# Optimization experiments

Measured on AMD Instinct MI355X. Metric: run time of the kernel, lower is better.

## Reference

```python
import jax, jax.numpy as jnp
import numpy as np

B, C, N, K = 8, 192, 3136, 9
COUT = 384


def setup_inputs() -> dict:
    key = jax.random.key(0)
    k1, k2, k3, k4 = jax.random.split(key, 4)
    x = jax.random.normal(k1, (B, C, N, 1), dtype=jnp.float32)
    edge_index = jax.random.randint(k2, (2, B, N, K), 0, N, dtype=jnp.int64)
    # 1x1 conv params: BasicConv([2C, COUT]) with bias, act='relu'
    W = jax.random.normal(k3, (COUT, 2 * C), dtype=jnp.float32) * (1.0 / np.sqrt(2 * C))
    b = jax.random.normal(k4, (COUT,), dtype=jnp.float32) * 0.01
    return {"x": x, "edge_index": edge_index, "W": W, "b": b}


def _gather(xs, idx):
    # xs: [B, C, N]; idx: [B, N, K] -> [B, C, N, K]
    return jax.vmap(lambda xb, ib: xb[:, ib])(xs, idx)


def reference(x, edge_index, W, b):
    xs = x[..., 0]                       # [B, C, N]
    x_i = _gather(xs, edge_index[1])     # [B, C, N, K] center features
    x_j = _gather(xs, edge_index[0])     # [B, C, N, K] neighbor features
    feat = jnp.concatenate([x_i, x_j - x_i], axis=1)  # [B, 2C, N, K]
    # 1x1 conv + bias + relu
    h = jnp.einsum('oi,bink->bonk', W, feat) + b[None, :, None, None]
    h = jax.nn.relu(h)                   # [B, COUT, N, K]
    return jnp.max(h, axis=-1, keepdims=True)  # [B, COUT, N, 1]
```

## Files before the change

### kernel.cpp

```cpp
#include <hip/hip_runtime.h>
#include <hip/hip_bf16.h>


#define Bb   8
#define Cc   192
#define Nn   3136
#define Kk   9
#define CO   384
#define TWOC 384
#define JTOT 768

typedef short  short8 __attribute__((ext_vector_type(8)));
typedef float  f32x4  __attribute__((ext_vector_type(4)));

__device__ __forceinline__ float bf2f(unsigned int u16) {
    union { unsigned int i; float f; } c;
    c.i = u16 << 16;
    return c.f;
}
__device__ __forceinline__ short f2bf(float f) {
    __hip_bfloat16 h = __float2bfloat16(f);
    short s; __builtin_memcpy(&s, &h, 2); return s;
}

__global__ __launch_bounds__(64) void detect(const unsigned short* __restrict__ xu,
                                             const int* __restrict__ ei,
                                             int* __restrict__ flags) {
    const int lane = threadIdx.x;
    unsigned int u = xu[2 * lane];
    int bige = (((u >> 7) & 0xFFu) >= 0x88u);
    unsigned long long bf = __ballot(bige);
    int oddnz = (ei[2 * lane + 1] != 0);
    unsigned long long bo = __ballot(oddnz);
    if (lane == 0) {
        flags[0] = (bf != 0ull) ? 1 : 0;
        flags[1] = (bo == 0ull) ? 1 : 0;
    }
}

__global__ __launch_bounds__(256) void prep_AT(const void* __restrict__ W_,
                                               short* __restrict__ A_Tb,
                                               const int* __restrict__ flags) {
    const int fp32 = flags[0];
    int t = blockIdx.x * 256 + threadIdx.x;
    if (t >= JTOT * Cc) return;
    int j = t / Cc;
    int c = t - j * Cc;
    int row = (j < CO) ? j : (j - CO);
    float w1, w2;
    if (fp32) {
        const float* W = (const float*)W_;
        w1 = W[row * TWOC + c];  w2 = W[row * TWOC + Cc + c];
    } else {
        const unsigned short* W = (const unsigned short*)W_;
        w1 = bf2f(W[row * TWOC + c]);  w2 = bf2f(W[row * TWOC + Cc + c]);
    }
    A_Tb[t] = f2bf((j < CO) ? (w1 - w2) : w2);
}

#define MT 64
#define NT 256
#define KT 32
#define LPAD 40

__global__ __launch_bounds__(256) void gemm_mfma(const void* __restrict__ x_,
                                                 const short* __restrict__ A_Tb,
                                                 short* __restrict__ U,
                                                 short* __restrict__ V,
                                                 const int* __restrict__ flags) {
    __shared__ short Asl[MT * LPAD];
    __shared__ short Bsl[NT * LPAD];

    const int fp32 = flags[0];
    const int n0 = blockIdx.x * MT;
    const int j0 = blockIdx.y * NT;
    const int b  = blockIdx.z;
    const int tid  = threadIdx.x;
    const int w    = tid >> 6;
    const int lane = tid & 63;
    const int col  = lane & 15;
    const int quad = lane >> 4;

    f32x4 acc[4][4];
#pragma unroll
    for (int i = 0; i < 4; ++i)
#pragma unroll
        for (int jf = 0; jf < 4; ++jf) acc[i][jf] = (f32x4)(0.0f);

    const int ac   = tid >> 3;
    const int aseg = tid & 7;

    for (int c0 = 0; c0 < Cc; c0 += KT) {
        if (fp32) {
            const float* xb = (const float*)x_ + ((size_t)b * Cc + c0 + ac) * Nn + n0 + aseg * 8;
            float4 v0 = *(const float4*)xb;
            float4 v1 = *(const float4*)(xb + 4);
            int nb = aseg * 8;
            Asl[(nb + 0) * LPAD + ac] = f2bf(v0.x);
            Asl[(nb + 1) * LPAD + ac] = f2bf(v0.y);
            Asl[(nb + 2) * LPAD + ac] = f2bf(v0.z);
            Asl[(nb + 3) * LPAD + ac] = f2bf(v0.w);
            Asl[(nb + 4) * LPAD + ac] = f2bf(v1.x);
            Asl[(nb + 5) * LPAD + ac] = f2bf(v1.y);
            Asl[(nb + 6) * LPAD + ac] = f2bf(v1.z);
            Asl[(nb + 7) * LPAD + ac] = f2bf(v1.w);
        } else {
            const unsigned short* xb = (const unsigned short*)x_ + ((size_t)b * Cc + c0 + ac) * Nn + n0 + aseg * 8;
            ushort4 u0 = *(const ushort4*)xb;
            ushort4 u1 = *(const ushort4*)(xb + 4);
            int nb = aseg * 8;
            Asl[(nb + 0) * LPAD + ac] = (short)u0.x;
            Asl[(nb + 1) * LPAD + ac] = (short)u0.y;
            Asl[(nb + 2) * LPAD + ac] = (short)u0.z;
            Asl[(nb + 3) * LPAD + ac] = (short)u0.w;
            Asl[(nb + 4) * LPAD + ac] = (short)u1.x;
            Asl[(nb + 5) * LPAD + ac] = (short)u1.y;
            Asl[(nb + 6) * LPAD + ac] = (short)u1.z;
            Asl[(nb + 7) * LPAD + ac] = (short)u1.w;
        }
        {
            const short8* src = (const short8*)(A_Tb + (size_t)(j0 + tid) * Cc + c0);
#pragma unroll
            for (int h = 0; h < 4; ++h)
                *(short8*)(&Bsl[tid * LPAD + h * 8]) = src[h];
        }
        __syncthreads();

        short8 bf[4];
#pragma unroll
        for (int jf = 0; jf < 4; ++jf)
            bf[jf] = *(const short8*)(&Bsl[(w * 64 + jf * 16 + col) * LPAD + quad * 8]);
#pragma unroll
        for (int fm = 0; fm < 4; ++fm) {
            short8 a = *(const short8*)(&Asl[(fm * 16 + col) * LPAD + quad * 8]);
#pragma unroll
            for (int jf = 0; jf < 4; ++jf)
                acc[fm][jf] = __builtin_amdgcn_mfma_f32_16x16x32_bf16(a, bf[jf], acc[fm][jf], 0, 0, 0);
        }
        __syncthreads();
    }

    const int jbase = j0 + w * 64;
#pragma unroll
    for (int fn = 0; fn < 4; ++fn) {
        int j = jbase + fn * 16 + col;
        short* dst; int jj;
        if (j < CO) { dst = U; jj = j; } else { dst = V; jj = j - CO; }
#pragma unroll
        for (int fm = 0; fm < 4; ++fm) {
#pragma unroll
            for (int r = 0; r < 4; ++r) {
                int n = n0 + fm * 16 + quad * 4 + r;
                dst[((size_t)(b * Nn + n)) * CO + jj] = f2bf(acc[fm][fn][r]);
            }
        }
    }
}

__global__ __launch_bounds__(384) void gather_max(const int* __restrict__ ei,
                                                  const short* __restrict__ U,
                                                  const short* __restrict__ V,
                                                  const void* __restrict__ bias_,
                                                  void* __restrict__ out_,
                                                  const int* __restrict__ flags) {
    __shared__ float sm[32][385];
    __shared__ int si0[32][Kk];
    __shared__ int si1[32][Kk];

    const int fp32 = flags[0];
    const int is64 = flags[1];
    const int bid = blockIdx.x;
    const int b  = bid & 7;
    const int n0 = (bid >> 3) * 32;
    const int tid = threadIdx.x;

    for (int s = tid; s < 32 * 2 * Kk; s += 384) {
        int ln = s / (2 * Kk);
        int slot = s - ln * (2 * Kk);
        int n = n0 + ln;
        size_t pos; int* dstp;
        if (slot < Kk) { pos = ((size_t)b * Nn + n) * Kk + slot;              dstp = &si0[ln][slot]; }
        else           { pos = ((size_t)(Bb + b) * Nn + n) * Kk + (slot - Kk); dstp = &si1[ln][slot - Kk]; }
        int v = is64 ? ei[2 * pos] : ei[pos];
        *dstp = (v < 0) ? 0 : (v >= Nn ? Nn - 1 : v);
    }
    __syncthreads();

    const int p    = tid % 192;
    const int half = tid / 192;
    const unsigned short* Ub = (const unsigned short*)U + (size_t)b * Nn * CO;
    const unsigned short* Vb = (const unsigned short*)V + (size_t)b * Nn * CO;

    float b0, b1;
    if (fp32) {
        b0 = ((const float*)bias_)[2 * p];
        b1 = ((const float*)bias_)[2 * p + 1];
    } else {
        b0 = bf2f(((const unsigned short*)bias_)[2 * p]);
        b1 = bf2f(((const unsigned short*)bias_)[2 * p + 1]);
    }

    for (int ln = half * 16; ln < half * 16 + 16; ++ln) {
        float m0 = -INFINITY, m1 = -INFINITY;
#pragma unroll
        for (int k = 0; k < Kk; ++k) {
            unsigned int uu = *(const unsigned int*)(Ub + (size_t)si1[ln][k] * CO + 2 * p);
            unsigned int vv = *(const unsigned int*)(Vb + (size_t)si0[ln][k] * CO + 2 * p);
            m0 = fmaxf(m0, bf2f(uu & 0xffffu) + bf2f(vv & 0xffffu));
            m1 = fmaxf(m1, bf2f(uu >> 16) + bf2f(vv >> 16));
        }
        sm[ln][2 * p]     = fmaxf(m0 + b0, 0.0f);
        sm[ln][2 * p + 1] = fmaxf(m1 + b1, 0.0f);
    }
    __syncthreads();

    const int g = tid >> 5, l = tid & 31;
    if (fp32) {
        float* op = (float*)out_;
#pragma unroll
        for (int oo = 0; oo < 32; ++oo) {
            int o = g * 32 + oo;
            op[((size_t)b * CO + o) * Nn + n0 + l] = sm[l][o];
        }
    } else {
        __hip_bfloat16* op = (__hip_bfloat16*)out_;
#pragma unroll
        for (int oo = 0; oo < 32; ++oo) {
            int o = g * 32 + oo;
            op[((size_t)b * CO + o) * Nn + n0 + l] = __float2bfloat16(sm[l][o]);
        }
    }
}

extern "C" void kernel_launch(void* const* d_in, const int* in_sizes, int n_in,
                              void* d_out, int out_size, void* d_ws, size_t ws_size,
                              hipStream_t stream) {
    const void* x  = d_in[0];
    const int*  ei = (const int*)d_in[1];
    const void* W  = d_in[2];
    const void* bs = d_in[3];

    char* ws = (char*)d_ws;
    int*   flags = (int*)ws;
    short* A_Tb  = (short*)(ws + 1024);
    short* U     = (short*)(ws + (1u << 20));
    short* V     = U + (size_t)Bb * Nn * CO;

    detect<<<1, 64, 0, stream>>>((const unsigned short*)x, ei, flags);

    prep_AT<<<(JTOT * Cc + 255) / 256, 256, 0, stream>>>(W, A_Tb, flags);

    dim3 g1(Nn / MT, JTOT / NT, Bb);
    gemm_mfma<<<g1, 256, 0, stream>>>(x, A_Tb, U, V, flags);

    gather_max<<<(Nn / 32) * Bb, 384, 0, stream>>>(ei, U, V, bs, d_out, flags);
}
```

Before: 140.5 us.

## Pre-transpose x to padded bf16 layout and split gather_max across output halves

```diff
diff --git a/kernel.cpp b/kernel.cpp
--- a/kernel.cpp
+++ b/kernel.cpp
@@ -9,6 +9,7 @@
 #define CO   384
 #define TWOC 384
 #define JTOT 768
+#define PADC 200
 
 typedef short  short8 __attribute__((ext_vector_type(8)));
 typedef float  f32x4  __attribute__((ext_vector_type(4)));
@@ -55,7 +56,48 @@
         const unsigned short* W = (const unsigned short*)W_;
         w1 = bf2f(W[row * TWOC + c]);  w2 = bf2f(W[row * TWOC + Cc + c]);
     }
-    A_Tb[t] = f2bf((j < CO) ? (w1 - w2) : w2);
+    A_Tb[(size_t)j * PADC + c] = f2bf((j < CO) ? (w1 - w2) : w2);
+}
+
+__global__ __launch_bounds__(256) void transpose_x(const void* __restrict__ x_,
+                                                   short* __restrict__ xT,
+                                                   const int* __restrict__ flags) {
+    __shared__ float s[64][33];
+    const int fp32 = flags[0];
+    const int n0 = blockIdx.x * 64;
+    const int c0 = blockIdx.y * 32;
+    const int b  = blockIdx.z;
+    const int t  = threadIdx.x;
+    const int cl   = t >> 3;
+    const int nseg = t & 7;
+
+    if (fp32) {
+        const float* p = (const float*)x_ + ((size_t)b * Cc + c0 + cl) * Nn + n0 + nseg * 8;
+        float4 v0 = *(const float4*)p;
+        float4 v1 = *(const float4*)(p + 4);
+        int nb = nseg * 8;
+        s[nb + 0][cl] = v0.x;  s[nb + 1][cl] = v0.y;
+        s[nb + 2][cl] = v0.z;  s[nb + 3][cl] = v0.w;
+        s[nb + 4][cl] = v1.x;  s[nb + 5][cl] = v1.y;
+        s[nb + 6][cl] = v1.z;  s[nb + 7][cl] = v1.w;
+    } else {
+        const unsigned short* p = (const unsigned short*)x_ + ((size_t)b * Cc + c0 + cl) * Nn + n0 + nseg * 8;
+        ushort4 u0 = *(const ushort4*)p;
+        ushort4 u1 = *(const ushort4*)(p + 4);
+        int nb = nseg * 8;
+        s[nb + 0][cl] = bf2f(u0.x);  s[nb + 1][cl] = bf2f(u0.y);
+        s[nb + 2][cl] = bf2f(u0.z);  s[nb + 3][cl] = bf2f(u0.w);
+        s[nb + 4][cl] = bf2f(u1.x);  s[nb + 5][cl] = bf2f(u1.y);
+        s[nb + 6][cl] = bf2f(u1.z);  s[nb + 7][cl] = bf2f(u1.w);
+    }
+    __syncthreads();
+
+    const int nl = t >> 2;
+    const int cs = t & 3;
+    short8 o;
+#pragma unroll
+    for (int i = 0; i < 8; ++i) o[i] = f2bf(s[nl][cs * 8 + i]);
+    *(short8*)(xT + ((size_t)b * Nn + n0 + nl) * PADC + c0 + cs * 8) = o;
 }
 
 #define MT 64
@@ -63,15 +105,13 @@
 #define KT 32
 #define LPAD 40
 
-__global__ __launch_bounds__(256) void gemm_mfma(const void* __restrict__ x_,
+__global__ __launch_bounds__(256) void gemm_mfma(const short* __restrict__ xT,
                                                  const short* __restrict__ A_Tb,
                                                  short* __restrict__ U,
-                                                 short* __restrict__ V,
-                                                 const int* __restrict__ flags) {
+                                                 short* __restrict__ V) {
     __shared__ short Asl[MT * LPAD];
     __shared__ short Bsl[NT * LPAD];
 
-    const int fp32 = flags[0];
     const int n0 = blockIdx.x * MT;
     const int j0 = blockIdx.y * NT;
     const int b  = blockIdx.z;
@@ -87,42 +127,17 @@
 #pragma unroll
         for (int jf = 0; jf < 4; ++jf) acc[i][jf] = (f32x4)(0.0f);
 
-    const int ac   = tid >> 3;
-    const int aseg = tid & 7;
+    const int ar = tid >> 2;
+    const int ag = tid & 3;
 
     for (int c0 = 0; c0 < Cc; c0 += KT) {
-        if (fp32) {
-            const float* xb = (const float*)x_ + ((size_t)b * Cc + c0 + ac) * Nn + n0 + aseg * 8;
-            float4 v0 = *(const float4*)xb;
-            float4 v1 = *(const float4*)(xb + 4);
-            int nb = aseg * 8;
-            Asl[(nb + 0) * LPAD + ac] = f2bf(v0.x);
-            Asl[(nb + 1) * LPAD + ac] = f2bf(v0.y);
-            Asl[(nb + 2) * LPAD + ac] = f2bf(v0.z);
-            Asl[(nb + 3) * LPAD + ac] = f2bf(v0.w);
-            Asl[(nb + 4) * LPAD + ac] = f2bf(v1.x);
-            Asl[(nb + 5) * LPAD + ac] = f2bf(v1.y);
-            Asl[(nb + 6) * LPAD + ac] = f2bf(v1.z);
-            Asl[(nb + 7) * LPAD + ac] = f2bf(v1.w);
-        } else {
-            const unsigned short* xb = (const unsigned short*)x_ + ((size_t)b * Cc + c0 + ac) * Nn + n0 + aseg * 8;
-            ushort4 u0 = *(const ushort4*)xb;
-            ushort4 u1 = *(const ushort4*)(xb + 4);
-            int nb = aseg * 8;
-            Asl[(nb + 0) * LPAD + ac] = (short)u0.x;
-            Asl[(nb + 1) * LPAD + ac] = (short)u0.y;
-            Asl[(nb + 2) * LPAD + ac] = (short)u0.z;
-            Asl[(nb + 3) * LPAD + ac] = (short)u0.w;
-            Asl[(nb + 4) * LPAD + ac] = (short)u1.x;
-            Asl[(nb + 5) * LPAD + ac] = (short)u1.y;
-            Asl[(nb + 6) * LPAD + ac] = (short)u1.z;
-            Asl[(nb + 7) * LPAD + ac] = (short)u1.w;
-        }
-        {
-            const short8* src = (const short8*)(A_Tb + (size_t)(j0 + tid) * Cc + c0);
-#pragma unroll
-            for (int h = 0; h < 4; ++h)
-                *(short8*)(&Bsl[tid * LPAD + h * 8]) = src[h];
+        *(short8*)(Asl + ar * LPAD + ag * 8) =
+            *(const short8*)(xT + ((size_t)b * Nn + n0 + ar) * PADC + c0 + ag * 8);
+#pragma unroll
+        for (int h = 0; h < 4; ++h) {
+            int row = h * 64 + ar;
+            *(short8*)(Bsl + row * LPAD + ag * 8) =
+                *(const short8*)(A_Tb + (size_t)(j0 + row) * PADC + c0 + ag * 8);
         }
         __syncthreads();
 
@@ -163,49 +178,52 @@
                                                   const void* __restrict__ bias_,
                                                   void* __restrict__ out_,
                                                   const int* __restrict__ flags) {
-    __shared__ float sm[32][385];
+    __shared__ float sm[32][193];
     __shared__ int si0[32][Kk];
     __shared__ int si1[32][Kk];
 
     const int fp32 = flags[0];
     const int is64 = flags[1];
-    const int bid = blockIdx.x;
-    const int b  = bid & 7;
-    const int n0 = (bid >> 3) * 32;
-    const int tid = threadIdx.x;
+    const int bid  = blockIdx.x;
+    const int b    = bid & 7;
+    const int rest = bid >> 3;
+    const int half = rest / 98;
+    const int n0   = (rest % 98) * 32;
+    const int tid  = threadIdx.x;
 
     for (int s = tid; s < 32 * 2 * Kk; s += 384) {
         int ln = s / (2 * Kk);
         int slot = s - ln * (2 * Kk);
         int n = n0 + ln;
         size_t pos; int* dstp;
-        if (slot < Kk) { pos = ((size_t)b * Nn + n) * Kk + slot;              dstp = &si0[ln][slot]; }
+        if (slot < Kk) { pos = ((size_t)b * Nn + n) * Kk + slot;               dstp = &si0[ln][slot]; }
         else           { pos = ((size_t)(Bb + b) * Nn + n) * Kk + (slot - Kk); dstp = &si1[ln][slot - Kk]; }
         int v = is64 ? ei[2 * pos] : ei[pos];
         *dstp = (v < 0) ? 0 : (v >= Nn ? Nn - 1 : v);
     }
     __syncthreads();
 
-    const int p    = tid % 192;
-    const int half = tid / 192;
+    const int p   = tid % 96;
+    const int seg = tid / 96;
+    const int och = half * 192 + 2 * p;
     const unsigned short* Ub = (const unsigned short*)U + (size_t)b * Nn * CO;
     const unsigned short* Vb = (const unsigned short*)V + (size_t)b * Nn * CO;
 
     float b0, b1;
     if (fp32) {
-        b0 = ((const float*)bias_)[2 * p];
-        b1 = ((const float*)bias_)[2 * p + 1];
-    } else {
-        b0 = bf2f(((const unsigned short*)bias_)[2 * p]);
-        b1 = bf2f(((const unsigned short*)bias_)[2 * p + 1]);
-    }
-
-    for (int ln = half * 16; ln < half * 16 + 16; ++ln) {
+        b0 = ((const float*)bias_)[och];
+        b1 = ((const float*)bias_)[och + 1];
+    } else {
+        b0 = bf2f(((const unsigned short*)bias_)[och]);
+        b1 = bf2f(((const unsigned short*)bias_)[och + 1]);
+    }
+
+    for (int ln = seg * 8; ln < seg * 8 + 8; ++ln) {
         float m0 = -INFINITY, m1 = -INFINITY;
 #pragma unroll
         for (int k = 0; k < Kk; ++k) {
-            unsigned int uu = *(const unsigned int*)(Ub + (size_t)si1[ln][k] * CO + 2 * p);
-            unsigned int vv = *(const unsigned int*)(Vb + (size_t)si0[ln][k] * CO + 2 * p);
+            unsigned int uu = *(const unsigned int*)(Ub + (size_t)si1[ln][k] * CO + och);
+            unsigned int vv = *(const unsigned int*)(Vb + (size_t)si0[ln][k] * CO + och);
             m0 = fmaxf(m0, bf2f(uu & 0xffffu) + bf2f(vv & 0xffffu));
             m1 = fmaxf(m1, bf2f(uu >> 16) + bf2f(vv >> 16));
         }
@@ -218,16 +236,18 @@
     if (fp32) {
         float* op = (float*)out_;
 #pragma unroll
-        for (int oo = 0; oo < 32; ++oo) {
-            int o = g * 32 + oo;
-            op[((size_t)b * CO + o) * Nn + n0 + l] = sm[l][o];
+        for (int rr = 0; rr < 16; ++rr) {
+            int ol = g * 16 + rr;
+            int o  = half * 192 + ol;
+            op[((size_t)b * CO + o) * Nn + n0 + l] = sm[l][ol];
         }
     } else {
         __hip_bfloat16* op = (__hip_bfloat16*)out_;
 #pragma unroll
-        for (int oo = 0; oo < 32; ++oo) {
-            int o = g * 32 + oo;
-            op[((size_t)b * CO + o) * Nn + n0 + l] = __float2bfloat16(sm[l][o]);
+        for (int rr = 0; rr < 16; ++rr) {
+            int ol = g * 16 + rr;
+            int o  = half * 192 + ol;
+            op[((size_t)b * CO + o) * Nn + n0 + l] = __float2bfloat16(sm[l][ol]);
         }
     }
 }
@@ -243,15 +263,19 @@
     char* ws = (char*)d_ws;
     int*   flags = (int*)ws;
     short* A_Tb  = (short*)(ws + 1024);
-    short* U     = (short*)(ws + (1u << 20));
+    short* xT    = (short*)(ws + (512u << 10));
+    short* U     = (short*)(ws + (16u << 20));
     short* V     = U + (size_t)Bb * Nn * CO;
 
     detect<<<1, 64, 0, stream>>>((const unsigned short*)x, ei, flags);
 
     prep_AT<<<(JTOT * Cc + 255) / 256, 256, 0, stream>>>(W, A_Tb, flags);
 
+    dim3 gt(Nn / 64, Cc / 32, Bb);
+    transpose_x<<<gt, 256, 0, stream>>>(x, xT, flags);
+
     dim3 g1(Nn / MT, JTOT / NT, Bb);
-    gemm_mfma<<<g1, 256, 0, stream>>>(x, A_Tb, U, V, flags);
-
-    gather_max<<<(Nn / 32) * Bb, 384, 0, stream>>>(ei, U, V, bs, d_out, flags);
-}
+    gemm_mfma<<<g1, 256, 0, stream>>>(xT, A_Tb, U, V);
+
+    gather_max<<<Bb * 2 * (Nn / 32), 384, 0, stream>>>(ei, U, V, bs, d_out, flags);
+}
```

Result: slower. 148.7 us (+5.8%).
